# Kernel tuning notes

Hardware: AMD Instinct MI355X
Metric: run time of the kernel (lower is better)

## Reference

```python
import math
import jax, jax.numpy as jnp
import numpy as np

N_NODES = 10000
N_EDGES = 160000
F_IN = 256
HID = 500
N_OUT = 100


def setup_inputs() -> dict:
    key = jax.random.key(0)
    ks = jax.random.split(key, 20)
    inp = {}
    inp['x'] = jax.random.normal(ks[0], (N_NODES, F_IN), jnp.float32)
    inp['edge_src'] = jax.random.randint(ks[1], (N_EDGES,), 0, N_NODES, jnp.int32)
    inp['edge_dst'] = jax.random.randint(ks[2], (N_EDGES,), 0, N_NODES, jnp.int32)
    inp['edge_weight'] = jax.random.uniform(ks[3], (N_EDGES,), jnp.float32)
    s1 = 1.0 / math.sqrt(F_IN)
    s2 = 1.0 / math.sqrt(HID)
    inp['W1_rel'] = jax.random.uniform(ks[4], (HID, F_IN), jnp.float32, -s1, s1)
    inp['b1'] = jax.random.uniform(ks[5], (HID,), jnp.float32, -s1, s1)
    inp['W1_root'] = jax.random.uniform(ks[6], (HID, F_IN), jnp.float32, -s1, s1)
    inp['p1_w'] = jax.random.uniform(ks[7], (HID,), jnp.float32, -s2, s2)
    inp['W2_rel'] = jax.random.uniform(ks[8], (HID, HID), jnp.float32, -s2, s2)
    inp['b2'] = jax.random.uniform(ks[9], (HID,), jnp.float32, -s2, s2)
    inp['W2_root'] = jax.random.uniform(ks[10], (HID, HID), jnp.float32, -s2, s2)
    inp['p2_w'] = jax.random.uniform(ks[11], (HID,), jnp.float32, -s2, s2)
    s3 = 1.0 / math.sqrt(1000)
    inp['lin1_W'] = jax.random.uniform(ks[12], (2000, 1000), jnp.float32, -s3, s3)
    inp['lin1_b'] = jax.random.uniform(ks[13], (2000,), jnp.float32, -s3, s3)
    s4 = 1.0 / math.sqrt(2000)
    inp['lin2_W'] = jax.random.uniform(ks[14], (4000, 2000), jnp.float32, -s4, s4)
    inp['lin2_b'] = jax.random.uniform(ks[15], (4000,), jnp.float32, -s4, s4)
    s5 = 1.0 / math.sqrt(4000)
    inp['lin3_W'] = jax.random.uniform(ks[16], (N_OUT, 4000), jnp.float32, -s5, s5)
    inp['lin3_b'] = jax.random.uniform(ks[17], (N_OUT,), jnp.float32, -s5, s5)
    return inp


def graph_conv(x, src, dst, w, W_rel, b_rel, W_root):
    # PyG GraphConv: out_i = W_rel @ sum_{j->i} w_ji * x_j + b + W_root @ x_i
    msg = x[src] * w[:, None]                              # [E, F]
    agg = jax.ops.segment_sum(msg, dst, num_segments=x.shape[0])
    return agg @ W_rel.T + b_rel + x @ W_root.T


def topk_pool(x, src, dst, w, p_w, ratio=0.5):
    # PyG TopKPooling: score = tanh(x @ p / ||p||); keep top-k; scale x by score.
    N = x.shape[0]
    k = int(math.ceil(ratio * N))
    score = jnp.tanh((x @ p_w) / jnp.linalg.norm(p_w))
    vals, perm = jax.lax.top_k(score, k)
    x_new = x[perm] * vals[:, None]
    # keep fixed-size edge list; dropped edges get weight 0 and point to node 0
    new_idx = jnp.zeros((N,), jnp.int32).at[perm].set(jnp.arange(k, dtype=jnp.int32))
    mask = jnp.zeros((N,), bool).at[perm].set(True)
    keep = mask[src] & mask[dst]
    src_new = jnp.where(keep, new_idx[src], 0)
    dst_new = jnp.where(keep, new_idx[dst], 0)
    w_new = jnp.where(keep, w, 0.0)
    return x_new, src_new, dst_new, w_new


def readout(x):
    # global max pool + global mean pool over the single graph -> [1, 2F]
    return jnp.concatenate([jnp.max(x, 0, keepdims=True), jnp.mean(x, 0, keepdims=True)], axis=1)


def reference(x, edge_src, edge_dst, edge_weight,
              W1_rel, b1, W1_root, p1_w,
              W2_rel, b2, W2_root, p2_w,
              lin1_W, lin1_b, lin2_W, lin2_b, lin3_W, lin3_b):
    h = jax.nn.relu(graph_conv(x, edge_src, edge_dst, edge_weight, W1_rel, b1, W1_root))
    h, s1, d1, w1 = topk_pool(h, edge_src, edge_dst, edge_weight, p1_w)
    x1 = readout(h)
    h = jax.nn.relu(graph_conv(h, s1, d1, w1, W2_rel, b2, W2_root))
    h, _, _, _ = topk_pool(h, s1, d1, w1, p2_w)
    x2 = readout(h)
    z = x1 + x2                                            # [1, 1000]
    z = jax.nn.relu(z @ lin1_W.T + lin1_b)
    z = jax.nn.relu(z @ lin2_W.T + lin2_b)                 # dropout is identity at eval
    return jax.nn.sigmoid(z @ lin3_W.T + lin3_b)
```

## Files before the change

### kernel.cpp

```cpp
#include <hip/hip_runtime.h>
#include <hip/hip_bf16.h>
#include <math.h>

#define NN1   10000
#define NE    160000
#define FIN   256
#define HID   500
#define K1    5000
#define NN2   5000
#define K2    2500

#define CSR_OFFS   0u
#define CSR_POS    10008u
#define CSR_EDGE   20008u
#define OFF_AGG    340016u
#define OFF_H      2900016u
#define OFF_XP2    (OFF_H + 2500000u)
#define OFF_SCP    7900016u
#define OFF_RK1    10410016u
#define OFF_Z      10432016u
#define OFF_T1     10433016u
#define OFF_T2     10435016u
#define OFF_INV    10439016u
#define OFF_CNT    10439024u
#define OFF_PM1    10639024u
#define OFF_PS1    10671024u
#define OFF_XB     10703024u
#define OFF_W1RB   11983024u
#define OFF_W1TB   12047024u
#define OFF_W2RB   12111024u
#define OFF_W2TB   12236024u
#define OFF_XP1B   12361024u
#define OFF_PM2    13611024u
#define OFF_PS2    13627024u
#define WS_FLOATS  13643024u

#define RCHUNK 500
#define ROSLAB1 64
#define ROSLAB2 32
#define RORPB   79

__device__ inline unsigned f2ord(float f) {
    unsigned u = __float_as_uint(f);
    return (u & 0x80000000u) ? ~u : (u | 0x80000000u);
}
__device__ inline unsigned long long rkey(float s, int j) {
    return ((unsigned long long)f2ord(s) << 32) | (unsigned)(0xFFFFFFFFu - (unsigned)j);
}
__device__ inline unsigned short bf16rn(float f) {
    unsigned u = __float_as_uint(f);
    u += 0x7FFFu + ((u >> 16) & 1u);
    return (unsigned short)(u >> 16);
}
__device__ inline float bf2f(unsigned short u) {
    return __uint_as_float((unsigned)u << 16);
}

typedef __attribute__((ext_vector_type(8))) short short8;
typedef __attribute__((ext_vector_type(4))) float floatx4;


__global__ __launch_bounds__(256) void k_prep(
    const float* __restrict__ x, unsigned short* __restrict__ xb,
    const float* __restrict__ w1r, unsigned short* __restrict__ w1rb,
    const float* __restrict__ w1t, unsigned short* __restrict__ w1tb,
    const float* __restrict__ w2r, unsigned short* __restrict__ w2rb,
    const float* __restrict__ w2t, unsigned short* __restrict__ w2tb,
    const float* __restrict__ p1, const float* __restrict__ p2,
    float* __restrict__ invn,
    const int* __restrict__ edst, int* __restrict__ pos) {
    __shared__ float red[256];
    int y = blockIdx.y;
    if (y < 5) {
        const float* s; unsigned short* d; int n;
        switch (y) {
            case 0: s = x;   d = xb;   n = NN1 * FIN; break;
            case 1: s = w1r; d = w1rb; n = HID * FIN; break;
            case 2: s = w1t; d = w1tb; n = HID * FIN; break;
            case 3: s = w2r; d = w2rb; n = HID * HID; break;
            default: s = w2t; d = w2tb; n = HID * HID; break;
        }
        int i = (blockIdx.x * 256 + threadIdx.x) * 4;
        if (i >= n) return;
        if (i + 3 < n) {
            float4 v = *(const float4*)(s + i);
            ushort4 o;
            o.x = bf16rn(v.x); o.y = bf16rn(v.y); o.z = bf16rn(v.z); o.w = bf16rn(v.w);
            *(ushort4*)(d + i) = o;
        } else {
            for (int q = 0; q < 4 && i + q < n; ++q) d[i + q] = bf16rn(s[i + q]);
        }
    } else if (y == 5) {
        if (blockIdx.x >= 2) return;
        const float* p = blockIdx.x ? p2 : p1;
        float s = 0.f;
        for (int i = threadIdx.x; i < HID; i += 256) { float v = p[i]; s += v * v; }
        red[threadIdx.x] = s; __syncthreads();
        for (int w = 128; w > 0; w >>= 1) {
            if (threadIdx.x < w) red[threadIdx.x] += red[threadIdx.x + w];
            __syncthreads();
        }
        if (threadIdx.x == 0) invn[blockIdx.x] = 1.0f / sqrtf(red[0]);
    } else {
        int e = blockIdx.x * 256 + threadIdx.x;
        if (e < NE) atomicAdd(&pos[edst[e]], 1);
    }
}

__global__ __launch_bounds__(1024) void k_scan(int* __restrict__ pos, int* __restrict__ offs) {
    __shared__ int tot[1024];
    int t = threadIdx.x;
    int base = t * 10;
    int loc[10]; int s = 0;
    #pragma unroll
    for (int q = 0; q < 10; ++q) {
        int v = (base + q < NN1) ? pos[base + q] : 0;
        loc[q] = s; s += v;
    }
    tot[t] = s; __syncthreads();
    for (int d = 1; d < 1024; d <<= 1) {
        int v = (t >= d) ? tot[t - d] : 0;
        __syncthreads();
        tot[t] += v;
        __syncthreads();
    }
    int excl = (t == 0) ? 0 : tot[t - 1];
    #pragma unroll
    for (int q = 0; q < 10; ++q)
        if (base + q < NN1) { int o = excl + loc[q]; offs[base + q] = o; pos[base + q] = o; }
    if (t == 1023) offs[NN1] = tot[1023];
}

__global__ void k_fill(const int* __restrict__ src, const int* __restrict__ dst,
                       const float* __restrict__ w, int* __restrict__ pos,
                       int2* __restrict__ ce) {
    int e = blockIdx.x * 256 + threadIdx.x;
    if (e >= NE) return;
    int slot = atomicAdd(&pos[dst[e]], 1);
    ce[slot] = make_int2(src[e], __float_as_int(w[e]));
}

__global__ __launch_bounds__(256) void k_gather1(
    const unsigned short* __restrict__ xb, const int* __restrict__ offs,
    const int2* __restrict__ ce, unsigned short* __restrict__ aggb) {
    int wave = (blockIdx.x * 256 + threadIdx.x) >> 6;
    int lane = threadIdx.x & 63;
    if (wave >= NN1) return;
    int b = offs[wave], e = offs[wave + 1];
    float4 acc = make_float4(0.f, 0.f, 0.f, 0.f);
    int2 nxt = (b < e) ? ce[b] : make_int2(0, 0);
    for (int p = b; p < e; ++p) {
        int2 cur = nxt;
        if (p + 1 < e) nxt = ce[p + 1];
        float we = __int_as_float(cur.y);
        ushort4 u = *(const ushort4*)(xb + (size_t)cur.x * FIN + lane * 4);
        acc.x += bf2f(u.x) * we; acc.y += bf2f(u.y) * we;
        acc.z += bf2f(u.z) * we; acc.w += bf2f(u.w) * we;
    }
    ushort4 o;
    o.x = bf16rn(acc.x); o.y = bf16rn(acc.y); o.z = bf16rn(acc.z); o.w = bf16rn(acc.w);
    *(ushort4*)(aggb + (size_t)wave * FIN + lane * 4) = o;
}

__global__ __launch_bounds__(256) void k_gather2(
    const unsigned short* __restrict__ Xb, const int* __restrict__ offs,
    const int2* __restrict__ ce, const int* __restrict__ rank,
    unsigned short* __restrict__ aggb) {
    int wave = (blockIdx.x * 256 + threadIdx.x) >> 6;
    int lane = threadIdx.x & 63;
    if (wave >= NN1) return;
    int rd = rank[wave];
    if (rd < 0) return;
    int b = offs[wave], e = offs[wave + 1];
    int c1 = 256 + lane * 4;
    float a0 = 0.f, a1 = 0.f, a2 = 0.f, a3 = 0.f;
    float b0 = 0.f, b1v = 0.f, b2 = 0.f, b3 = 0.f;
    int2 nxt = (b < e) ? ce[b] : make_int2(0, 0);
    for (int p = b; p < e; ++p) {
        int2 cur = nxt;
        if (p + 1 < e) nxt = ce[p + 1];
        int rs = rank[cur.x];
        if (rs < 0) continue;
        float we = __int_as_float(cur.y);
        const unsigned short* row = Xb + (size_t)rs * HID;
        ushort4 u = *(const ushort4*)(row + lane * 4);
        a0 += bf2f(u.x) * we; a1 += bf2f(u.y) * we;
        a2 += bf2f(u.z) * we; a3 += bf2f(u.w) * we;
        if (c1 < HID) {
            ushort4 u2 = *(const ushort4*)(row + c1);
            b0 += bf2f(u2.x) * we; b1v += bf2f(u2.y) * we;
            b2 += bf2f(u2.z) * we; b3 += bf2f(u2.w) * we;
        }
    }
    unsigned short* o = aggb + (size_t)rd * HID;
    ushort4 o1; o1.x = bf16rn(a0); o1.y = bf16rn(a1); o1.z = bf16rn(a2); o1.w = bf16rn(a3);
    *(ushort4*)(o + lane * 4) = o1;
    if (c1 < HID) {
        ushort4 o2; o2.x = bf16rn(b0); o2.y = bf16rn(b1v); o2.z = bf16rn(b2); o2.w = bf16rn(b3);
        *(ushort4*)(o + c1) = o2;
    }
}

__device__ inline short8 ld8g(const unsigned short* p, int gk, int K) {
    if (gk + 7 < K) return *(const short8*)p;
    unsigned short tmp[8] = {0,0,0,0,0,0,0,0};
    for (int q = 0; q < 8; ++q) if (gk + q < K) tmp[q] = p[q];
    return *(short8*)tmp;
}

#define GBK 64
#define APAD 72
__global__ __launch_bounds__(256) void k_gemm_bf16(
    const unsigned short* __restrict__ A1, const unsigned short* __restrict__ B1,
    const unsigned short* __restrict__ A2, const unsigned short* __restrict__ B2,
    const float* __restrict__ bias, const float* __restrict__ pv,
    unsigned short* __restrict__ C, float* __restrict__ scpart,
    int M, int N, int Ka, int Kb, int nbyRow) {
    int b = blockIdx.x;
    int xcd = b & 7, seq = b >> 3;
    int colT = seq & 7;
    int rowT = xcd + 8 * (seq >> 3);
    if (rowT >= nbyRow) return;
    int row0 = rowT * 64, col0 = colT * 64;

    __shared__ unsigned short As[64 * APAD];
    __shared__ unsigned short Bs[64 * APAD];
    int tid = threadIdx.x;
    int lane = tid & 63, wid = tid >> 6;
    int waveM = wid & 1, waveN = wid >> 1;
    int quad = lane >> 4, mrow = lane & 15;
    floatx4 acc[2][2] = {};

    int sr = tid >> 2;
    int sk = (tid & 3) * 16;

    int nka = (Ka + GBK - 1) / GBK;
    int nkb = (Kb + GBK - 1) / GBK;
    int niter = nka + nkb;

    short8 z8 = {0,0,0,0,0,0,0,0};
    short8 paA = z8, paB = z8, pbA = z8, pbB = z8;

    auto fetch = [&](const unsigned short* A, const unsigned short* B, int K, int k0) {
        int gr = row0 + sr, gn = col0 + sr, gk = k0 + sk;
        paA = z8; paB = z8; pbA = z8; pbB = z8;
        if (gr < M) {
            const unsigned short* p = A + (size_t)gr * K + gk;
            paA = ld8g(p, gk, K); paB = ld8g(p + 8, gk + 8, K);
        }
        if (gn < N) {
            const unsigned short* p = B + (size_t)gn * K + gk;
            pbA = ld8g(p, gk, K); pbB = ld8g(p + 8, gk + 8, K);
        }
    };

    fetch(A1, B1, Ka, 0);

    for (int it = 0; it < niter; ++it) {
        *(short8*)&As[sr * APAD + sk]     = paA;
        *(short8*)&As[sr * APAD + sk + 8] = paB;
        *(short8*)&Bs[sr * APAD + sk]     = pbA;
        *(short8*)&Bs[sr * APAD + sk + 8] = pbB;
        __syncthreads();
        if (it + 1 < niter) {
            int t = it + 1;
            int ph = (t >= nka);
            fetch(ph ? A2 : A1, ph ? B2 : B1, ph ? Kb : Ka, (ph ? t - nka : t) * GBK);
        }
        #pragma unroll
        for (int half = 0; half < 2; ++half) {
            int ko = half * 32 + quad * 8;
            short8 bfr[2];
            #pragma unroll
            for (int nt = 0; nt < 2; ++nt)
                bfr[nt] = *(short8*)&Bs[(waveN * 32 + nt * 16 + mrow) * APAD + ko];
            #pragma unroll
            for (int mt = 0; mt < 2; ++mt) {
                short8 afr = *(short8*)&As[(waveM * 32 + mt * 16 + mrow) * APAD + ko];
                #pragma unroll
                for (int nt = 0; nt < 2; ++nt)
                    acc[mt][nt] = __builtin_amdgcn_mfma_f32_16x16x32_bf16(
                        afr, bfr[nt], acc[mt][nt], 0, 0, 0);
            }
        }
        __syncthreads();
    }
    float ps[2][4] = {};
    #pragma unroll
    for (int nt = 0; nt < 2; ++nt) {
        int col = col0 + waveN * 32 + nt * 16 + mrow;
        if (col >= N) continue;
        float bv = bias[col];
        float pc = pv[col];
        #pragma unroll
        for (int mt = 0; mt < 2; ++mt) {
            int rbase = row0 + waveM * 32 + mt * 16 + quad * 4;
            #pragma unroll
            for (int r = 0; r < 4; ++r) {
                float v = fmaxf(acc[mt][nt][r] + bv, 0.f);
                int row = rbase + r;
                if (row < M) C[(size_t)row * N + col] = bf16rn(v);
                ps[mt][r] += v * pc;
            }
        }
    }
    int part = colT * 2 + waveN;
    #pragma unroll
    for (int mt = 0; mt < 2; ++mt)
        #pragma unroll
        for (int r = 0; r < 4; ++r) {
            float v = ps[mt][r];
            v += __shfl_xor(v, 1, 64); v += __shfl_xor(v, 2, 64);
            v += __shfl_xor(v, 4, 64); v += __shfl_xor(v, 8, 64);
            if (mrow == 0) {
                int row = row0 + waveM * 32 + mt * 16 + quad * 4 + r;
                if (row < M) scpart[(size_t)part * M + row] = v;
            }
        }
}

__global__ __launch_bounds__(256) void k_rank_partial(
    const float* __restrict__ scpart, int* __restrict__ cntp, int Nn) {
    __shared__ unsigned long long kj[RCHUNK];
    int j0 = blockIdx.y * RCHUNK;
    int jn = min(Nn - j0, RCHUNK);
    for (int t = threadIdx.x; t < jn; t += 256) {
        float s = 0.f;
        #pragma unroll
        for (int q = 0; q < 16; ++q) s += scpart[(size_t)q * Nn + j0 + t];
        kj[t] = rkey(s, j0 + t);
    }
    __syncthreads();
    int i = blockIdx.x * 256 + threadIdx.x;
    if (i >= Nn) return;
    float si = 0.f;
    #pragma unroll
    for (int q = 0; q < 16; ++q) si += scpart[(size_t)q * Nn + i];
    unsigned long long ki = rkey(si, i);
    int c = 0;
    #pragma unroll 4
    for (int q = 0; q < jn; ++q)
        c += (kj[q] > ki) ? 1 : 0;
    cntp[(size_t)blockIdx.y * Nn + i] = c;
}

__global__ __launch_bounds__(128) void k_gather_pool(
    const unsigned short* __restrict__ Hb, const float* __restrict__ scpart,
    const float* __restrict__ invn,
    const int* __restrict__ cntp, int Nn, int nchunk, int kk,
    int* __restrict__ rank_out, unsigned short* __restrict__ Xb) {
    __shared__ int csum[128];
    __shared__ float ssum[128];
    __shared__ int rsh;
    __shared__ float scsh;
    int i = blockIdx.x;
    int c = 0;
    for (int q = threadIdx.x; q < nchunk; q += 128) c += cntp[(size_t)q * Nn + i];
    float s = (threadIdx.x < 16) ? scpart[(size_t)threadIdx.x * Nn + i] : 0.f;
    csum[threadIdx.x] = c; ssum[threadIdx.x] = s;
    __syncthreads();
    if (threadIdx.x == 0) {
        int t = 0;
        int lim = (nchunk < 128) ? nchunk : 128;
        for (int q = 0; q < lim; ++q) t += csum[q];
        float st = 0.f;
        for (int q = 0; q < 16; ++q) st += ssum[q];
        int r = (t < kk) ? t : -1;
        if (rank_out) rank_out[i] = r;
        rsh = r;
        scsh = tanhf(st * invn[0]);
    }
    __syncthreads();
    int r = rsh;
    if (r < 0) return;
    float sc = scsh;
    int cc = threadIdx.x;
    if (cc < HID / 4) {
        ushort4 u = *(const ushort4*)(Hb + (size_t)i * HID + cc * 4);
        ushort4 o;
        o.x = bf16rn(bf2f(u.x) * sc); o.y = bf16rn(bf2f(u.y) * sc);
        o.z = bf16rn(bf2f(u.z) * sc); o.w = bf16rn(bf2f(u.w) * sc);
        *(ushort4*)(Xb + (size_t)r * HID + cc * 4) = o;
    }
}

__global__ __launch_bounds__(256) void k_readout_slab(
    const unsigned short* __restrict__ X, int rows, int rpb,
    float* __restrict__ pmax, float* __restrict__ psum) {
    __shared__ float4 lmx[4][64];
    __shared__ float4 lsm[4][64];
    int lane = threadIdx.x & 63;
    int rgrp = threadIdx.x >> 6;
    int c4 = blockIdx.x * 64 + lane;
    int r0 = blockIdx.y * rpb;
    int r1 = min(rows, r0 + rpb);
    float4 mx = make_float4(-INFINITY, -INFINITY, -INFINITY, -INFINITY);
    float4 sm = make_float4(0.f, 0.f, 0.f, 0.f);
    if (c4 < HID / 4) {
        for (int r = r0 + rgrp; r < r1; r += 4) {
            ushort4 u = *(const ushort4*)(X + (size_t)r * HID + c4 * 4);
            float vx = bf2f(u.x), vy = bf2f(u.y), vz = bf2f(u.z), vw = bf2f(u.w);
            mx.x = fmaxf(mx.x, vx); mx.y = fmaxf(mx.y, vy);
            mx.z = fmaxf(mx.z, vz); mx.w = fmaxf(mx.w, vw);
            sm.x += vx; sm.y += vy; sm.z += vz; sm.w += vw;
        }
    }
    lmx[rgrp][lane] = mx; lsm[rgrp][lane] = sm;
    __syncthreads();
    if (rgrp == 0 && c4 < HID / 4) {
        #pragma unroll
        for (int g = 1; g < 4; ++g) {
            float4 m2 = lmx[g][lane], s2 = lsm[g][lane];
            mx.x = fmaxf(mx.x, m2.x); mx.y = fmaxf(mx.y, m2.y);
            mx.z = fmaxf(mx.z, m2.z); mx.w = fmaxf(mx.w, m2.w);
            sm.x += s2.x; sm.y += s2.y; sm.z += s2.z; sm.w += s2.w;
        }
        *(float4*)(pmax + (size_t)blockIdx.y * HID + c4 * 4) = mx;
        *(float4*)(psum + (size_t)blockIdx.y * HID + c4 * 4) = sm;
    }
}

__global__ __launch_bounds__(64) void k_combine_all(
    const float* __restrict__ pm1, const float* __restrict__ ps1, int ns1,
    const float* __restrict__ pm2, const float* __restrict__ ps2, int ns2,
    float* __restrict__ z) {
    int j = blockIdx.x * 64 + threadIdx.x;
    if (j >= HID) return;
    float m1 = -INFINITY, s1 = 0.f;
    for (int s = 0; s < ns1; ++s) {
        m1 = fmaxf(m1, pm1[(size_t)s * HID + j]);
        s1 += ps1[(size_t)s * HID + j];
    }
    float m2 = -INFINITY, s2 = 0.f;
    for (int s = 0; s < ns2; ++s) {
        m2 = fmaxf(m2, pm2[(size_t)s * HID + j]);
        s2 += ps2[(size_t)s * HID + j];
    }
    z[j] = m1 + m2;
    z[HID + j] = s1 * (1.0f / (float)K1) + s2 * (1.0f / (float)K2);
}

__global__ __launch_bounds__(256) void k_mv(
    const float* __restrict__ v, const float* __restrict__ W,
    const float* __restrict__ bias, float* __restrict__ y,
    int rowsN, int K, int act) {
    int wave = (blockIdx.x * 256 + threadIdx.x) >> 6;
    int lane = threadIdx.x & 63;
    if (wave >= rowsN) return;
    const float* wr = W + (size_t)wave * K;
    float s = 0.f;
    for (int c = lane * 4; c < K; c += 256) {
        float4 a = *(const float4*)(wr + c);
        float4 xv = *(const float4*)(v + c);
        s += a.x * xv.x + a.y * xv.y + a.z * xv.z + a.w * xv.w;
    }
    for (int off = 32; off > 0; off >>= 1) s += __shfl_down(s, off, 64);
    if (lane == 0) {
        float r = s + bias[wave];
        y[wave] = (act == 0) ? fmaxf(r, 0.f) : 1.f / (1.f + expf(-r));
    }
}

extern "C" void kernel_launch(void* const* d_in, const int* in_sizes, int n_in,
                              void* d_out, int out_size, void* d_ws, size_t ws_size,
                              hipStream_t stream) {
    const float* x      = (const float*)d_in[0];
    const int*   esrc   = (const int*)d_in[1];
    const int*   edst   = (const int*)d_in[2];
    const float* ew     = (const float*)d_in[3];
    const float* W1_rel = (const float*)d_in[4];
    const float* b1     = (const float*)d_in[5];
    const float* W1_root= (const float*)d_in[6];
    const float* p1     = (const float*)d_in[7];
    const float* W2_rel = (const float*)d_in[8];
    const float* b2     = (const float*)d_in[9];
    const float* W2_root= (const float*)d_in[10];
    const float* p2     = (const float*)d_in[11];
    const float* l1W    = (const float*)d_in[12];
    const float* l1b    = (const float*)d_in[13];
    const float* l2W    = (const float*)d_in[14];
    const float* l2b    = (const float*)d_in[15];
    const float* l3W    = (const float*)d_in[16];
    const float* l3b    = (const float*)d_in[17];
    float* out = (float*)d_out;
    float* ws  = (float*)d_ws;

    if (ws_size < (size_t)WS_FLOATS * sizeof(float)) return;

    int*            offs  = (int*)(ws + CSR_OFFS);
    int*            pos   = (int*)(ws + CSR_POS);
    int2*           ce    = (int2*)(ws + CSR_EDGE);
    unsigned short* aggb  = (unsigned short*)(ws + OFF_AGG);
    unsigned short* hb    = (unsigned short*)(ws + OFF_H);
    unsigned short* xp2b  = (unsigned short*)(ws + OFF_XP2);
    float*          scp   = ws + OFF_SCP;
    int*            rk1   = (int*)(ws + OFF_RK1);
    float*          zbuf  = ws + OFF_Z;
    float*          t1    = ws + OFF_T1;
    float*          t2    = ws + OFF_T2;
    float*          invn  = ws + OFF_INV;
    int*            cntp  = (int*)(ws + OFF_CNT);
    float*          pm1   = ws + OFF_PM1;
    float*          ps1   = ws + OFF_PS1;
    float*          pm2   = ws + OFF_PM2;
    float*          ps2   = ws + OFF_PS2;
    unsigned short* xb    = (unsigned short*)(ws + OFF_XB);
    unsigned short* w1rb  = (unsigned short*)(ws + OFF_W1RB);
    unsigned short* w1tb  = (unsigned short*)(ws + OFF_W1TB);
    unsigned short* w2rb  = (unsigned short*)(ws + OFF_W2RB);
    unsigned short* w2tb  = (unsigned short*)(ws + OFF_W2TB);
    unsigned short* xp1b  = (unsigned short*)(ws + OFF_XP1B);

    hipMemsetAsync(pos, 0, NN1 * sizeof(int), stream);
    k_prep<<<dim3(2500, 7), 256, 0, stream>>>(
        x, xb, W1_rel, w1rb, W1_root, w1tb, W2_rel, w2rb, W2_root, w2tb,
        p1, p2, invn, edst, pos);
    k_scan<<<1, 1024, 0, stream>>>(pos, offs);
    k_fill<<<(NE + 255) / 256, 256, 0, stream>>>(esrc, edst, ew, pos, ce);

    k_gather1<<<(NN1 * 64 + 255) / 256, 256, 0, stream>>>(xb, offs, ce, aggb);
    {
        int nby = (NN1 + 63) / 64;
        int nblk = 64 * ((nby + 7) / 8);
        k_gemm_bf16<<<nblk, 256, 0, stream>>>(
            aggb, w1rb, xb, w1tb, b1, p1, hb, scp, NN1, HID, FIN, FIN, nby);
    }

    k_rank_partial<<<dim3((NN1 + 255) / 256, NN1 / RCHUNK), 256, 0, stream>>>(scp, cntp, NN1);
    k_gather_pool<<<NN1, 128, 0, stream>>>(hb, scp, invn + 0, cntp, NN1, NN1 / RCHUNK, K1,
                                           rk1, xp1b);
    k_readout_slab<<<dim3(2, ROSLAB1), 256, 0, stream>>>(xp1b, K1, RORPB, pm1, ps1);

    k_gather2<<<(NN1 * 64 + 255) / 256, 256, 0, stream>>>(xp1b, offs, ce, rk1, aggb);
    {
        int nby = (NN2 + 63) / 64;
        int nblk = 64 * ((nby + 7) / 8);
        k_gemm_bf16<<<nblk, 256, 0, stream>>>(
            aggb, w2rb, xp1b, w2tb, b2, p2, hb, scp, NN2, HID, HID, HID, nby);
    }

    k_rank_partial<<<dim3((NN2 + 255) / 256, NN2 / RCHUNK), 256, 0, stream>>>(scp, cntp, NN2);
    k_gather_pool<<<NN2, 128, 0, stream>>>(hb, scp, invn + 1, cntp, NN2, NN2 / RCHUNK, K2,
                                           (int*)nullptr, xp2b);
    k_readout_slab<<<dim3(2, ROSLAB2), 256, 0, stream>>>(xp2b, K2, RORPB, pm2, ps2);
    k_combine_all<<<(HID + 63) / 64, 64, 0, stream>>>(pm1, ps1, ROSLAB1, pm2, ps2, ROSLAB2, zbuf);

    k_mv<<<(2000 * 64) / 256, 256, 0, stream>>>(zbuf, l1W, l1b, t1, 2000, 1000, 0);
    k_mv<<<(4000 * 64) / 256, 256, 0, stream>>>(t1, l2W, l2b, t2, 4000, 2000, 0);
    k_mv<<<(100 * 64) / 256, 256, 0, stream>>>(t2, l3W, l3b, out, 100, 4000, 1);
}
```

Before: 329.1 us.

## Double-buffer GEMM LDS tiles with XOR swizzle and unroll gather1 by two

The bf16 MFMA GEMM now uses two LDS buffers and keeps global prefetches two iterations ahead. The aim is to drop one __syncthreads per k-step and overlap loads with MFMA work. The padded LDS layout is replaced by an XOR swizzle on 16-byte chunks to avoid bank conflicts while using less padding. The layer-1 gather loop processes two edges per iteration with separate accumulators to expose more memory-level parallelism. This raises register and LDS use and needs correct synchronisation between buffers.

```diff
diff --git a/kernel.cpp b/kernel.cpp
--- a/kernel.cpp
+++ b/kernel.cpp
@@ -147,18 +147,29 @@
     int lane = threadIdx.x & 63;
     if (wave >= NN1) return;
     int b = offs[wave], e = offs[wave + 1];
-    float4 acc = make_float4(0.f, 0.f, 0.f, 0.f);
-    int2 nxt = (b < e) ? ce[b] : make_int2(0, 0);
-    for (int p = b; p < e; ++p) {
-        int2 cur = nxt;
-        if (p + 1 < e) nxt = ce[p + 1];
-        float we = __int_as_float(cur.y);
-        ushort4 u = *(const ushort4*)(xb + (size_t)cur.x * FIN + lane * 4);
-        acc.x += bf2f(u.x) * we; acc.y += bf2f(u.y) * we;
-        acc.z += bf2f(u.z) * we; acc.w += bf2f(u.w) * we;
+    float4 a0 = make_float4(0.f, 0.f, 0.f, 0.f);
+    float4 a1 = make_float4(0.f, 0.f, 0.f, 0.f);
+    int p = b;
+    for (; p + 1 < e; p += 2) {
+        int2 e0 = ce[p], e1 = ce[p + 1];
+        float w0 = __int_as_float(e0.y), w1 = __int_as_float(e1.y);
+        ushort4 u0 = *(const ushort4*)(xb + (size_t)e0.x * FIN + lane * 4);
+        ushort4 u1 = *(const ushort4*)(xb + (size_t)e1.x * FIN + lane * 4);
+        a0.x += bf2f(u0.x) * w0; a0.y += bf2f(u0.y) * w0;
+        a0.z += bf2f(u0.z) * w0; a0.w += bf2f(u0.w) * w0;
+        a1.x += bf2f(u1.x) * w1; a1.y += bf2f(u1.y) * w1;
+        a1.z += bf2f(u1.z) * w1; a1.w += bf2f(u1.w) * w1;
+    }
+    if (p < e) {
+        int2 e0 = ce[p];
+        float w0 = __int_as_float(e0.y);
+        ushort4 u0 = *(const ushort4*)(xb + (size_t)e0.x * FIN + lane * 4);
+        a0.x += bf2f(u0.x) * w0; a0.y += bf2f(u0.y) * w0;
+        a0.z += bf2f(u0.z) * w0; a0.w += bf2f(u0.w) * w0;
     }
     ushort4 o;
-    o.x = bf16rn(acc.x); o.y = bf16rn(acc.y); o.z = bf16rn(acc.z); o.w = bf16rn(acc.w);
+    o.x = bf16rn(a0.x + a1.x); o.y = bf16rn(a0.y + a1.y);
+    o.z = bf16rn(a0.z + a1.z); o.w = bf16rn(a0.w + a1.w);
     *(ushort4*)(aggb + (size_t)wave * FIN + lane * 4) = o;
 }
 
@@ -209,7 +220,6 @@
 }
 
 #define GBK 64
-#define APAD 72
 __global__ __launch_bounds__(256) void k_gemm_bf16(
     const unsigned short* __restrict__ A1, const unsigned short* __restrict__ B1,
     const unsigned short* __restrict__ A2, const unsigned short* __restrict__ B2,
@@ -223,16 +233,21 @@
     if (rowT >= nbyRow) return;
     int row0 = rowT * 64, col0 = colT * 64;
 
-    __shared__ unsigned short As[64 * APAD];
-    __shared__ unsigned short Bs[64 * APAD];
+    __shared__ unsigned short As[2][64 * 64];
+    __shared__ unsigned short Bs[2][64 * 64];
     int tid = threadIdx.x;
     int lane = tid & 63, wid = tid >> 6;
     int waveM = wid & 1, waveN = wid >> 1;
     int quad = lane >> 4, mrow = lane & 15;
+    int m7 = mrow & 7;
     floatx4 acc[2][2] = {};
 
     int sr = tid >> 2;
-    int sk = (tid & 3) * 16;
+    int ca = (tid & 3) * 2;
+    int s7 = sr & 7;
+    int c0 = (ca ^ s7) * 8;
+    int c1 = ((ca + 1) ^ s7) * 8;
+    int sbase = sr * 64;
 
     int nka = (Ka + GBK - 1) / GBK;
     int nkb = (Kb + GBK - 1) / GBK;
@@ -241,8 +256,13 @@
     short8 z8 = {0,0,0,0,0,0,0,0};
     short8 paA = z8, paB = z8, pbA = z8, pbB = z8;
 
-    auto fetch = [&](const unsigned short* A, const unsigned short* B, int K, int k0) {
-        int gr = row0 + sr, gn = col0 + sr, gk = k0 + sk;
+    auto fetch = [&](int t) {
+        int ph = (t >= nka);
+        const unsigned short* A = ph ? A2 : A1;
+        const unsigned short* B = ph ? B2 : B1;
+        int K = ph ? Kb : Ka;
+        int gk = (ph ? t - nka : t) * GBK + ca * 8;
+        int gr = row0 + sr, gn = col0 + sr;
         paA = z8; paB = z8; pbA = z8; pbB = z8;
         if (gr < M) {
             const unsigned short* p = A + (size_t)gr * K + gk;
@@ -253,30 +273,33 @@
             pbA = ld8g(p, gk, K); pbB = ld8g(p + 8, gk + 8, K);
         }
     };
-
-    fetch(A1, B1, Ka, 0);
+    auto commit = [&](int buf) {
+        *(short8*)&As[buf][sbase + c0] = paA;
+        *(short8*)&As[buf][sbase + c1] = paB;
+        *(short8*)&Bs[buf][sbase + c0] = pbA;
+        *(short8*)&Bs[buf][sbase + c1] = pbB;
+    };
+
+    fetch(0);
+    commit(0);
+    if (niter > 1) fetch(1);
+    __syncthreads();
 
     for (int it = 0; it < niter; ++it) {
-        *(short8*)&As[sr * APAD + sk]     = paA;
-        *(short8*)&As[sr * APAD + sk + 8] = paB;
-        *(short8*)&Bs[sr * APAD + sk]     = pbA;
-        *(short8*)&Bs[sr * APAD + sk + 8] = pbB;
-        __syncthreads();
-        if (it + 1 < niter) {
-            int t = it + 1;
-            int ph = (t >= nka);
-            fetch(ph ? A2 : A1, ph ? B2 : B1, ph ? Kb : Ka, (ph ? t - nka : t) * GBK);
-        }
+        int cur = it & 1;
+        if (it + 1 < niter) commit(cur ^ 1);
+        if (it + 2 < niter) fetch(it + 2);
         #pragma unroll
         for (int half = 0; half < 2; ++half) {
-            int ko = half * 32 + quad * 8;
+            int qc = half * 4 + quad;
+            int qoff = (qc ^ m7) * 8;
             short8 bfr[2];
             #pragma unroll
             for (int nt = 0; nt < 2; ++nt)
-                bfr[nt] = *(short8*)&Bs[(waveN * 32 + nt * 16 + mrow) * APAD + ko];
+                bfr[nt] = *(short8*)&Bs[cur][(waveN * 32 + nt * 16 + mrow) * 64 + qoff];
             #pragma unroll
             for (int mt = 0; mt < 2; ++mt) {
-                short8 afr = *(short8*)&As[(waveM * 32 + mt * 16 + mrow) * APAD + ko];
+                short8 afr = *(short8*)&As[cur][(waveM * 32 + mt * 16 + mrow) * 64 + qoff];
                 #pragma unroll
                 for (int nt = 0; nt < 2; ++nt)
                     acc[mt][nt] = __builtin_amdgcn_mfma_f32_16x16x32_bf16(
```

Measured after the change: 328.5 us, median of 2. Within noise of the previous version (-0.2%).
